# Performance work log

Measured on AMD Instinct MI355X. Metric: run time of the kernel, lower is better.

## Reference

```python
import jax, jax.numpy as jnp
import numpy as np

N, E = 50000, 800000
IN_C, HID, HEADS, NUM_CLASSES = 256, 64, 4, 10
LRELU_SLOPE = 0.2
LN_EPS = 1e-5


def setup_inputs() -> dict:
    key = jax.random.key(0)
    ks = jax.random.split(key, 12)
    HC = HEADS * HID
    glorot = lambda k, shp: jax.random.normal(k, shp, jnp.float32) * np.sqrt(2.0 / (shp[0] + shp[-1]))
    return {
        "x": jax.random.normal(ks[0], (N, IN_C), jnp.float32),
        "edge_index": jax.random.randint(ks[1], (2, E), 0, N, jnp.int64),
        "edge_weight": jax.random.uniform(ks[2], (E, 1), jnp.float32),
        "W": glorot(ks[3], (IN_C, HC)),
        "att_src": glorot(ks[4], (1, HEADS, HID)),
        "att_dst": glorot(ks[5], (1, HEADS, HID)),
        "att_edge": glorot(ks[6], (1, HEADS, HID)),
        "W_edge": glorot(ks[7], (1, HC)),
        "bias": jnp.zeros((HC,), jnp.float32),
        "ln_gamma": jnp.ones((HC,), jnp.float32),
        "ln_beta": jnp.zeros((HC,), jnp.float32),
        "fc_W": glorot(ks[8], (HC, NUM_CLASSES)),
        "fc_b": jnp.zeros((NUM_CLASSES,), jnp.float32),
    }


def reference(x, edge_index, edge_weight, W, att_src, att_dst, att_edge,
              W_edge, bias, ln_gamma, ln_beta, fc_W, fc_b):
    n = x.shape[0]
    src, dst = edge_index[0], edge_index[1]

    # GATConv: linear projection -> [N, H, C]
    xh = (x @ W).reshape(n, HEADS, HID)
    a_src = jnp.sum(xh * att_src, axis=-1)  # [N, H]
    a_dst = jnp.sum(xh * att_dst, axis=-1)  # [N, H]

    # edge feature projection (edge_dim=1) -> per-edge attention term
    eh = (edge_weight @ W_edge).reshape(-1, HEADS, HID)  # [E, H, C]
    a_edge = jnp.sum(eh * att_edge, axis=-1)             # [E, H]

    alpha = a_src[src] + a_dst[dst] + a_edge             # [E, H]
    alpha = jax.nn.leaky_relu(alpha, LRELU_SLOPE)

    # segment softmax over incoming edges of each destination node
    amax = jax.ops.segment_max(alpha, dst, num_segments=n)  # [N, H]
    amax = jnp.where(jnp.isfinite(amax), amax, 0.0)
    ex = jnp.exp(alpha - amax[dst])
    esum = jax.ops.segment_sum(ex, dst, num_segments=n)     # [N, H]
    attn = ex / (esum[dst] + 1e-16)                          # [E, H]

    # message = gathered source features weighted by attention; scatter-add
    msg = xh[src] * attn[:, :, None]                          # [E, H, C]
    out = jax.ops.segment_sum(msg, dst, num_segments=n)      # [N, H, C]
    out = out.reshape(n, HEADS * HID) + bias                  # concat heads

    # LayerNorm + ReLU (dropout is identity in eval) + Linear head
    mu = jnp.mean(out, axis=-1, keepdims=True)
    var = jnp.mean(jnp.square(out - mu), axis=-1, keepdims=True)
    out = (out - mu) * jax.lax.rsqrt(var + LN_EPS) * ln_gamma + ln_beta
    out = jax.nn.relu(out)
    return out @ fc_W + fc_b
```

## Files before the change

### kernel.cpp

```cpp
#include <hip/hip_runtime.h>
#include <hip/hip_bf16.h>

static constexpr int HEADS = 4;
static constexpr int HID   = 64;
static constexpr int HC    = 256;
static constexpr int NCLS  = 10;

typedef short    bf16x8 __attribute__((ext_vector_type(8)));
typedef _Float16 f16x8  __attribute__((ext_vector_type(8)));
typedef _Float16 f16x4  __attribute__((ext_vector_type(4)));
typedef float    f32x4  __attribute__((ext_vector_type(4)));

__device__ inline unsigned short f2bf(float f) {
    union { float f; unsigned u; } c; c.f = f;
    unsigned r = (c.u + 0x7fff + ((c.u >> 16) & 1)) >> 16;
    return (unsigned short)r;
}
__device__ inline unsigned short f2h(float f) {
    _Float16 h = (_Float16)f; unsigned short u; __builtin_memcpy(&u, &h, 2); return u;
}
__device__ inline float h2f(unsigned short u) {
    _Float16 h; __builtin_memcpy(&h, &u, 2); return (float)h;
}

__global__ void prep_kernel(const float* __restrict__ We, const float* __restrict__ attE,
                            float* __restrict__ cE, const float* __restrict__ W,
                            unsigned short* __restrict__ Wt, const float* __restrict__ fcW,
                            unsigned short* __restrict__ fcWh) {
    int b = blockIdx.x, t = threadIdx.x;
    if (b == 0) {
        float p = We[t] * attE[t];
#pragma unroll
        for (int d = 32; d; d >>= 1) p += __shfl_xor(p, d, 64);
        if ((t & 63) == 0) cE[t >> 6] = p;
    } else if (b <= 256) {
        int k = b - 1;
        Wt[t * 256 + k] = f2bf(W[k * 256 + t]);
    } else {
        int j = b - 257;
        unsigned short v = 0;
        if (j < NCLS) v = f2h(fcW[t * NCLS + j]);
        fcWh[j * 256 + t] = v;
    }
}

__global__ __launch_bounds__(256) void gemm_mfma(const float* __restrict__ X,
                                                 const unsigned short* __restrict__ Bt,
                                                 unsigned short* __restrict__ XHh, int M) {
    __shared__ alignas(16) unsigned short As[128][40];
    __shared__ alignas(16) unsigned short Bs[128][40];
    const int tid = threadIdx.x;
    const int lane = tid & 63, wid = tid >> 6;
    const int wr = wid >> 1, wc = wid & 1;
    const int bm = blockIdx.x * 128, bn = blockIdx.y * 128;
    const int fr = lane & 15, kg = lane >> 4;

    f32x4 acc[4][4] = {};

    for (int k0 = 0; k0 < 256; k0 += 32) {
        __syncthreads();
#pragma unroll
        for (int ss = 0; ss < 4; ++ss) {
            int idx = tid + (ss << 8);
            int row = idx >> 3, seg = idx & 7;
            int grow = bm + row;
            float4 av = make_float4(0.f, 0.f, 0.f, 0.f);
            if (grow < M) av = *(const float4*)&X[(size_t)grow * 256 + k0 + seg * 4];
            ushort4 ab = make_ushort4(f2bf(av.x), f2bf(av.y), f2bf(av.z), f2bf(av.w));
            *(ushort4*)&As[row][seg * 4] = ab;
        }
#pragma unroll
        for (int qq = 0; qq < 2; ++qq) {
            int q = tid + (qq << 8);
            int row = q >> 2, part = q & 3;
            const ushort4* bp = (const ushort4*)&Bt[(size_t)(bn + row) * 256 + k0 + part * 8];
            *(ushort4*)&Bs[row][part * 8]     = bp[0];
            *(ushort4*)&Bs[row][part * 8 + 4] = bp[1];
        }
        __syncthreads();

        bf16x8 af[4], bf[4];
#pragma unroll
        for (int i = 0; i < 4; ++i)
            af[i] = *(const bf16x8*)&As[wr * 64 + i * 16 + fr][kg * 8];
#pragma unroll
        for (int j = 0; j < 4; ++j)
            bf[j] = *(const bf16x8*)&Bs[wc * 64 + j * 16 + fr][kg * 8];
#pragma unroll
        for (int i = 0; i < 4; ++i)
#pragma unroll
            for (int j = 0; j < 4; ++j)
                acc[i][j] = __builtin_amdgcn_mfma_f32_16x16x32_bf16(af[i], bf[j], acc[i][j], 0, 0, 0);
    }

#pragma unroll
    for (int i = 0; i < 4; ++i) {
#pragma unroll
        for (int j = 0; j < 4; ++j) {
            int col = bn + wc * 64 + j * 16 + fr;
#pragma unroll
            for (int r = 0; r < 4; ++r) {
                int row = bm + wr * 64 + i * 16 + kg * 4 + r;
                if (row < M) XHh[(size_t)row * 256 + col] = f2h(acc[i][j][r]);
            }
        }
    }
}

__global__ __launch_bounds__(256) void attn_coef(const unsigned short* __restrict__ xhh,
                                                 const float* __restrict__ attS,
                                                 const float* __restrict__ attD,
                                                 float* __restrict__ a_src,
                                                 float* __restrict__ a_dst,
                                                 int Nn) {
    int wid = threadIdx.x >> 6, lane = threadIdx.x & 63;
    int n = blockIdx.x * 4 + wid;
    if (n >= Nn) return;
    ushort4 xv = *(const ushort4*)&xhh[(size_t)n * HC + lane * 4];
    float x0 = h2f(xv.x), x1 = h2f(xv.y), x2 = h2f(xv.z), x3 = h2f(xv.w);
    float4 sv = *(const float4*)&attS[lane * 4];
    float4 dv = *(const float4*)&attD[lane * 4];
    float ps = x0 * sv.x + x1 * sv.y + x2 * sv.z + x3 * sv.w;
    float pd = x0 * dv.x + x1 * dv.y + x2 * dv.z + x3 * dv.w;
#pragma unroll
    for (int d = 1; d < 16; d <<= 1) {
        ps += __shfl_xor(ps, d, 64);
        pd += __shfl_xor(pd, d, 64);
    }
    if ((lane & 15) == 0) {
        a_src[n * 4 + (lane >> 4)] = ps;
        a_dst[n * 4 + (lane >> 4)] = pd;
    }
}

__global__ void hist_kernel(const int* __restrict__ dst, int* __restrict__ deg,
                            int* __restrict__ rank, int E) {
    int e = blockIdx.x * 256 + threadIdx.x;
    if (e < E) rank[e] = atomicAdd(&deg[dst[e]], 1);
}

__global__ __launch_bounds__(1024) void scan1(const int* __restrict__ deg,
                                              int* __restrict__ row_start,
                                              int* __restrict__ bsum, int n) {
    __shared__ int wsum[16];
    const int tid = threadIdx.x, lane = tid & 63, wid = tid >> 6;
    int i = blockIdx.x * 1024 + tid;
    int v = (i < n) ? ((deg[i] + 3) & ~3) : 0;
    int incl = v;
#pragma unroll
    for (int d = 1; d < 64; d <<= 1) {
        int t = __shfl_up(incl, d, 64);
        if (lane >= d) incl += t;
    }
    if (lane == 63) wsum[wid] = incl;
    __syncthreads();
    if (tid < 16) {
        int w = wsum[tid];
#pragma unroll
        for (int d = 1; d < 16; d <<= 1) {
            int t = __shfl_up(w, d, 16);
            if (tid >= d) w += t;
        }
        wsum[tid] = w;
    }
    __syncthreads();
    int waveoff = wid ? wsum[wid - 1] : 0;
    if (i < n) row_start[i] = waveoff + incl - v;
    if (tid == 1023) bsum[blockIdx.x] = waveoff + incl;
}

__global__ __launch_bounds__(1024) void scan23(int* __restrict__ row_start,
                                               const int* __restrict__ bsum,
                                               const int* __restrict__ deg,
                                               int* __restrict__ srcs, int n, int nb) {
    __shared__ int pref[64];
    const int tid = threadIdx.x;
    if (tid < 64) {
        int v = (tid < nb) ? bsum[tid] : 0;
#pragma unroll
        for (int d = 1; d < 64; d <<= 1) {
            int t = __shfl_up(v, d, 64);
            if (tid >= d) v += t;
        }
        pref[tid] = v;
    }
    __syncthreads();
    int add = blockIdx.x ? pref[blockIdx.x - 1] : 0;
    int i = blockIdx.x * 1024 + tid;
    if (i < n) {
        int v = row_start[i] + add;
        row_start[i] = v;
        int dn = deg[i];
        int pd = (dn + 3) & ~3;
        for (int s = dn; s < pd; ++s) srcs[v + s] = 0;
    }
    if (i == n) row_start[n] = pref[nb - 1];
}

__global__ void scatter_sw(const int* __restrict__ src, const int* __restrict__ dst,
                           const float* __restrict__ ew,
                           const int* __restrict__ row_start, const int* __restrict__ rank,
                           int* __restrict__ srcs, float* __restrict__ ews, int E) {
    int e = blockIdx.x * 256 + threadIdx.x;
    if (e >= E) return;
    int pos = row_start[dst[e]] + rank[e];
    srcs[pos] = src[e];
    ews[pos] = ew[e];
}

__global__ __launch_bounds__(256) void p_pass(
    const int* __restrict__ row_start, const int* __restrict__ deg,
    const int* __restrict__ srcs, const float* __restrict__ ews,
    const float* __restrict__ a_src, const float* __restrict__ a_dst,
    const float* __restrict__ cE, float* __restrict__ pq, int Nn) {
    const int wid = threadIdx.x >> 6, lane = threadIdx.x & 63;
    const int n = blockIdx.x * 4 + wid;
    if (n >= Nn) return;
    const int rs = row_start[n];
    const int dn = deg[n];
    const int pd = (dn + 3) & ~3;
    const int slot0 = lane >> 2, h = lane & 3;
    const float adn = a_dst[n * 4 + h];
    const float ceh = cE[h];
    for (int s = slot0; s < pd; s += 16) {
        int pos = rs + s;
        float p = 0.f;
        if (s < dn) {
            int sv = srcs[pos];
            float w = ews[pos];
            float a = a_src[sv * 4 + h] + adn + ceh * w;
            a = fmaxf(a, 0.2f * a);
            p = __expf(a);
        }
        pq[(size_t)(pos >> 2) * 16 + h * 4 + (pos & 3)] = p;
    }
}

__global__ __launch_bounds__(256) void gat_main(
    const unsigned short* __restrict__ xhh, const int* __restrict__ row_start,
    const int* __restrict__ deg, const int* __restrict__ srcs,
    const float* __restrict__ pq, const float* __restrict__ bias,
    const float* __restrict__ gamma, const float* __restrict__ beta,
    unsigned short* __restrict__ yh, int Nn) {
    const int lane = threadIdx.x & 63, wid = threadIdx.x >> 6;
    const int n = blockIdx.x * 4 + wid;
    if (n >= Nn) return;
    const int myh = lane >> 4;
    const int rs = row_start[n];
    const int dn = deg[n];
    const int nfull = dn >> 2, rem = dn & 3;
    const unsigned short* xl = xhh + (size_t)lane * 4;

    f32x4 acc = {0.f, 0.f, 0.f, 0.f};
    float psum = 0.f;

#define LOADMETA(c, S, P)                                                     \
    S = *(const int4*)&srcs[rs + (c) * 4];                                    \
    P = *(const float4*)&pq[((size_t)((rs >> 2) + (c))) * 16 + myh * 4];
#define GATHER(S, X0, X1, X2, X3)                                             \
    X0 = *(const f16x4*)(xl + (size_t)__builtin_amdgcn_readfirstlane((S).x) * HC); \
    X1 = *(const f16x4*)(xl + (size_t)__builtin_amdgcn_readfirstlane((S).y) * HC); \
    X2 = *(const f16x4*)(xl + (size_t)__builtin_amdgcn_readfirstlane((S).z) * HC); \
    X3 = *(const f16x4*)(xl + (size_t)__builtin_amdgcn_readfirstlane((S).w) * HC);
#define COMPUTE(P, X0, X1, X2, X3)                                            \
    psum += ((P).x + (P).y) + ((P).z + (P).w);                                \
    acc[0] = fmaf((P).x, (float)(X0).x, acc[0]);                              \
    acc[1] = fmaf((P).x, (float)(X0).y, acc[1]);                              \
    acc[2] = fmaf((P).x, (float)(X0).z, acc[2]);                              \
    acc[3] = fmaf((P).x, (float)(X0).w, acc[3]);                              \
    acc[0] = fmaf((P).y, (float)(X1).x, acc[0]);                              \
    acc[1] = fmaf((P).y, (float)(X1).y, acc[1]);                              \
    acc[2] = fmaf((P).y, (float)(X1).z, acc[2]);                              \
    acc[3] = fmaf((P).y, (float)(X1).w, acc[3]);                              \
    acc[0] = fmaf((P).z, (float)(X2).x, acc[0]);                              \
    acc[1] = fmaf((P).z, (float)(X2).y, acc[1]);                              \
    acc[2] = fmaf((P).z, (float)(X2).z, acc[2]);                              \
    acc[3] = fmaf((P).z, (float)(X2).w, acc[3]);                              \
    acc[0] = fmaf((P).w, (float)(X3).x, acc[0]);                              \
    acc[1] = fmaf((P).w, (float)(X3).y, acc[1]);                              \
    acc[2] = fmaf((P).w, (float)(X3).z, acc[2]);                              \
    acc[3] = fmaf((P).w, (float)(X3).w, acc[3]);

    if (nfull > 0) {
        int4 s0, sN = {0, 0, 0, 0}, s2 = {0, 0, 0, 0};
        float4 pC, pN = {0.f, 0.f, 0.f, 0.f}, p2 = {0.f, 0.f, 0.f, 0.f};
        f16x4 g0, g1, g2, g3;
        LOADMETA(0, s0, pC);
        GATHER(s0, g0, g1, g2, g3);
        if (nfull > 1) { LOADMETA(1, sN, pN); }
        for (int c = 0; c < nfull; ++c) {
            f16x4 h0, h1, h2, h3;
            if (c + 1 < nfull) { GATHER(sN, h0, h1, h2, h3); }
            if (c + 2 < nfull) { LOADMETA(c + 2, s2, p2); }
            COMPUTE(pC, g0, g1, g2, g3);
            pC = pN; pN = p2; sN = s2;
            g0 = h0; g1 = h1; g2 = h2; g3 = h3;
        }
    }
    if (rem) {
        int4 s; float4 p;
        LOADMETA(nfull, s, p);
        p.w = 0.f;
        if (rem < 3) p.z = 0.f;
        if (rem < 2) p.y = 0.f;
        int b0 = __builtin_amdgcn_readfirstlane(s.x);
        int b1 = rem > 1 ? __builtin_amdgcn_readfirstlane(s.y) : b0;
        int b2 = rem > 2 ? __builtin_amdgcn_readfirstlane(s.z) : b0;
        f16x4 x0 = *(const f16x4*)(xl + (size_t)b0 * HC);
        f16x4 x1 = *(const f16x4*)(xl + (size_t)b1 * HC);
        f16x4 x2 = *(const f16x4*)(xl + (size_t)b2 * HC);
        COMPUTE(p, x0, x1, x2, x0);
    }
#undef LOADMETA
#undef GATHER
#undef COMPUTE

    float rin = 1.f / (psum + 1e-16f);

    float4 bv = *(const float4*)&bias[lane * 4];
    float v0 = acc[0] * rin + bv.x;
    float v1 = acc[1] * rin + bv.y;
    float v2 = acc[2] * rin + bv.z;
    float v3 = acc[3] * rin + bv.w;

    float s1 = v0 + v1 + v2 + v3;
    float s2v = v0 * v0 + v1 * v1 + v2 * v2 + v3 * v3;
#pragma unroll
    for (int d = 1; d < 64; d <<= 1) {
        s1 += __shfl_xor(s1, d, 64);
        s2v += __shfl_xor(s2v, d, 64);
    }
    float mu = s1 * (1.f / 256.f);
    float var = s2v * (1.f / 256.f) - mu * mu;
    float rstd = rsqrtf(var + 1e-5f);
    float4 gv = *(const float4*)&gamma[lane * 4];
    float4 btv = *(const float4*)&beta[lane * 4];
    float y0 = fmaxf((v0 - mu) * rstd * gv.x + btv.x, 0.f);
    float y1 = fmaxf((v1 - mu) * rstd * gv.y + btv.y, 0.f);
    float y2 = fmaxf((v2 - mu) * rstd * gv.z + btv.z, 0.f);
    float y3 = fmaxf((v3 - mu) * rstd * gv.w + btv.w, 0.f);

    f16x4 yv;
    yv.x = (_Float16)y0; yv.y = (_Float16)y1; yv.z = (_Float16)y2; yv.w = (_Float16)y3;
    *(f16x4*)&yh[(size_t)n * HC + lane * 4] = yv;
}

__global__ __launch_bounds__(256) void fc_gemm(const unsigned short* __restrict__ yh,
                                               const unsigned short* __restrict__ fcWh,
                                               const float* __restrict__ fcb,
                                               float* __restrict__ out, int M) {
    const int lane = threadIdx.x & 63, wid = threadIdx.x >> 6;
    const int rowbase = blockIdx.x * 256 + wid * 64;
    const int fr = lane & 15, kg = lane >> 4;
    f32x4 acc[4] = {};
#pragma unroll
    for (int k0 = 0; k0 < 256; k0 += 32) {
        f16x8 bfr = *(const f16x8*)&fcWh[fr * 256 + k0 + kg * 8];
#pragma unroll
        for (int i = 0; i < 4; ++i) {
            int row = rowbase + i * 16 + fr;
            f16x8 afr = {};
            if (row < M) afr = *(const f16x8*)&yh[(size_t)row * 256 + k0 + kg * 8];
            acc[i] = __builtin_amdgcn_mfma_f32_16x16x32_f16(afr, bfr, acc[i], 0, 0, 0);
        }
    }
    if (fr < NCLS) {
        float bb = fcb[fr];
#pragma unroll
        for (int i = 0; i < 4; ++i) {
#pragma unroll
            for (int r = 0; r < 4; ++r) {
                int row = rowbase + i * 16 + kg * 4 + r;
                if (row < M) out[(size_t)row * NCLS + fr] = acc[i][r] + bb;
            }
        }
    }
}

extern "C" void kernel_launch(void* const* d_in, const int* in_sizes, int n_in,
                              void* d_out, int out_size, void* d_ws, size_t ws_size,
                              hipStream_t stream) {
    const float* x    = (const float*)d_in[0];
    const int*   ei   = (const int*)d_in[1];
    const float* ew   = (const float*)d_in[2];
    const float* W    = (const float*)d_in[3];
    const float* attS = (const float*)d_in[4];
    const float* attD = (const float*)d_in[5];
    const float* attE = (const float*)d_in[6];
    const float* We   = (const float*)d_in[7];
    const float* bias = (const float*)d_in[8];
    const float* gam  = (const float*)d_in[9];
    const float* bet  = (const float*)d_in[10];
    const float* fcW  = (const float*)d_in[11];
    const float* fcb  = (const float*)d_in[12];
    float* out = (float*)d_out;

    const int Nn = in_sizes[0] / HC;
    const int E  = in_sizes[1] / 2;
    const int* src = ei;
    const int* dst = ei + E;
    const int nb = (Nn + 1023) / 1024;
    const int EpMax = E + 4 * Nn;

    char* ws = (char*)d_ws;
    size_t off = 0;
    auto alloc = [&](size_t bytes) { void* p = ws + off; off = (off + bytes + 255) & ~size_t(255); return p; };
    unsigned short* xhh  = (unsigned short*)alloc((size_t)Nn * HC * 2);
    unsigned short* yh   = (unsigned short*)alloc((size_t)Nn * HC * 2);
    unsigned short* wt   = (unsigned short*)alloc((size_t)HC * HC * 2);
    unsigned short* fcWh = (unsigned short*)alloc((size_t)16 * HC * 2);
    float* a_srcb    = (float*)alloc((size_t)Nn * 4 * 4);
    float* a_dstb    = (float*)alloc((size_t)Nn * 4 * 4);
    float* cE        = (float*)alloc(256);
    int*   row_start = (int*)  alloc((size_t)(Nn + 1) * 4);
    int*   deg       = (int*)  alloc((size_t)Nn * 4);
    int*   bsum      = (int*)  alloc((size_t)nb * 4);
    int*   rank      = (int*)  alloc((size_t)E * 4);
    int*   srcs      = (int*)  alloc((size_t)EpMax * 4 + 256);
    float* ews       = (float*)alloc((size_t)EpMax * 4 + 256);
    float* pq        = (float*)alloc((size_t)EpMax * 16 + 1024);
    (void)ws_size;

    hipMemsetAsync(deg, 0, (size_t)Nn * 4, stream);

    prep_kernel<<<273, 256, 0, stream>>>(We, attE, cE, W, wt, fcW, fcWh);

    dim3 g((Nn + 127) / 128, 2);
    gemm_mfma<<<g, 256, 0, stream>>>(x, wt, xhh, Nn);

    attn_coef<<<(Nn + 3) / 4, 256, 0, stream>>>(xhh, attS, attD, a_srcb, a_dstb, Nn);
    hist_kernel<<<(E + 255) / 256, 256, 0, stream>>>(dst, deg, rank, E);
    scan1<<<nb, 1024, 0, stream>>>(deg, row_start, bsum, Nn);
    scan23<<<nb, 1024, 0, stream>>>(row_start, bsum, deg, srcs, Nn, nb);
    scatter_sw<<<(E + 255) / 256, 256, 0, stream>>>(src, dst, ew, row_start, rank,
                                                    srcs, ews, E);
    p_pass<<<(Nn + 3) / 4, 256, 0, stream>>>(row_start, deg, srcs, ews,
                                             a_srcb, a_dstb, cE, pq, Nn);
    gat_main<<<(Nn + 3) / 4, 256, 0, stream>>>(xhh, row_start, deg, srcs, pq,
                                               bias, gam, bet, yh, Nn);
    fc_gemm<<<(Nn + 255) / 256, 256, 0, stream>>>(yh, fcWh, fcb, out, Nn);
}
```

Measured before the change: 208.0 us.

## Split GAT aggregation across two waves per node and pack edge records

```diff
diff --git a/kernel.cpp b/kernel.cpp
--- a/kernel.cpp
+++ b/kernel.cpp
@@ -26,7 +26,8 @@
 __global__ void prep_kernel(const float* __restrict__ We, const float* __restrict__ attE,
                             float* __restrict__ cE, const float* __restrict__ W,
                             unsigned short* __restrict__ Wt, const float* __restrict__ fcW,
-                            unsigned short* __restrict__ fcWh) {
+                            unsigned short* __restrict__ fcWh, int* __restrict__ deg,
+                            int Nn) {
     int b = blockIdx.x, t = threadIdx.x;
     if (b == 0) {
         float p = We[t] * attE[t];
@@ -36,11 +37,14 @@
     } else if (b <= 256) {
         int k = b - 1;
         Wt[t * 256 + k] = f2bf(W[k * 256 + t]);
-    } else {
+    } else if (b <= 272) {
         int j = b - 257;
         unsigned short v = 0;
         if (j < NCLS) v = f2h(fcW[t * NCLS + j]);
         fcWh[j * 256 + t] = v;
+    } else {
+        int i = (b - 273) * 256 + t;
+        if (i < Nn) deg[i] = 0;
     }
 }
 
@@ -172,7 +176,7 @@
 __global__ __launch_bounds__(1024) void scan23(int* __restrict__ row_start,
                                                const int* __restrict__ bsum,
                                                const int* __restrict__ deg,
-                                               int* __restrict__ srcs, int n, int nb) {
+                                               int2* __restrict__ sew, int n, int nb) {
     __shared__ int pref[64];
     const int tid = threadIdx.x;
     if (tid < 64) {
@@ -192,7 +196,7 @@
         row_start[i] = v;
         int dn = deg[i];
         int pd = (dn + 3) & ~3;
-        for (int s = dn; s < pd; ++s) srcs[v + s] = 0;
+        for (int s = dn; s < pd; ++s) sew[v + s] = make_int2(0, 0);
     }
     if (i == n) row_start[n] = pref[nb - 1];
 }
@@ -200,19 +204,18 @@
 __global__ void scatter_sw(const int* __restrict__ src, const int* __restrict__ dst,
                            const float* __restrict__ ew,
                            const int* __restrict__ row_start, const int* __restrict__ rank,
-                           int* __restrict__ srcs, float* __restrict__ ews, int E) {
+                           int2* __restrict__ sew, int E) {
     int e = blockIdx.x * 256 + threadIdx.x;
     if (e >= E) return;
     int pos = row_start[dst[e]] + rank[e];
-    srcs[pos] = src[e];
-    ews[pos] = ew[e];
+    sew[pos] = make_int2(src[e], __float_as_int(ew[e]));
 }
 
 __global__ __launch_bounds__(256) void p_pass(
     const int* __restrict__ row_start, const int* __restrict__ deg,
-    const int* __restrict__ srcs, const float* __restrict__ ews,
-    const float* __restrict__ a_src, const float* __restrict__ a_dst,
-    const float* __restrict__ cE, float* __restrict__ pq, int Nn) {
+    const int2* __restrict__ sew, const float* __restrict__ a_src,
+    const float* __restrict__ a_dst, const float* __restrict__ cE,
+    int* __restrict__ srcs, float* __restrict__ pq, int Nn) {
     const int wid = threadIdx.x >> 6, lane = threadIdx.x & 63;
     const int n = blockIdx.x * 4 + wid;
     if (n >= Nn) return;
@@ -224,39 +227,44 @@
     const float ceh = cE[h];
     for (int s = slot0; s < pd; s += 16) {
         int pos = rs + s;
+        int2 r = sew[pos];
         float p = 0.f;
         if (s < dn) {
-            int sv = srcs[pos];
-            float w = ews[pos];
-            float a = a_src[sv * 4 + h] + adn + ceh * w;
+            float a = a_src[r.x * 4 + h] + adn + ceh * __int_as_float(r.y);
             a = fmaxf(a, 0.2f * a);
             p = __expf(a);
         }
+        if (h == 0) srcs[pos] = r.x;
         pq[(size_t)(pos >> 2) * 16 + h * 4 + (pos & 3)] = p;
     }
 }
 
 __global__ __launch_bounds__(256) void gat_main(
     const unsigned short* __restrict__ xhh, const int* __restrict__ row_start,
-    const int* __restrict__ deg, const int* __restrict__ srcs,
-    const float* __restrict__ pq, const float* __restrict__ bias,
-    const float* __restrict__ gamma, const float* __restrict__ beta,
-    unsigned short* __restrict__ yh, int Nn) {
+    const int* __restrict__ srcs, const float* __restrict__ pq,
+    const float* __restrict__ bias, const float* __restrict__ gamma,
+    const float* __restrict__ beta, unsigned short* __restrict__ yh, int Nn) {
+    __shared__ alignas(16) f32x4 s_acc[2][64];
+    __shared__ float s_ps[2][64];
+
     const int lane = threadIdx.x & 63, wid = threadIdx.x >> 6;
-    const int n = blockIdx.x * 4 + wid;
-    if (n >= Nn) return;
+    const int nslot = wid >> 1, sub = wid & 1;
+    const int n = blockIdx.x * 2 + nslot;
     const int myh = lane >> 4;
-    const int rs = row_start[n];
-    const int dn = deg[n];
-    const int nfull = dn >> 2, rem = dn & 3;
     const unsigned short* xl = xhh + (size_t)lane * 4;
 
     f32x4 acc = {0.f, 0.f, 0.f, 0.f};
     float psum = 0.f;
 
+    if (n < Nn) {
+        const int rs = row_start[n], re = row_start[n + 1];
+        const int rs4 = rs >> 2;
+        const int G = (re - rs) >> 2;
+        const int myG = (G - sub + 1) >> 1;
+
 #define LOADMETA(c, S, P)                                                     \
-    S = *(const int4*)&srcs[rs + (c) * 4];                                    \
-    P = *(const float4*)&pq[((size_t)((rs >> 2) + (c))) * 16 + myh * 4];
+    S = *(const int4*)&srcs[(rs4 + (c)) * 4];                                 \
+    P = *(const float4*)&pq[((size_t)(rs4 + (c))) * 16 + myh * 4];
 #define GATHER(S, X0, X1, X2, X3)                                             \
     X0 = *(const f16x4*)(xl + (size_t)__builtin_amdgcn_readfirstlane((S).x) * HC); \
     X1 = *(const f16x4*)(xl + (size_t)__builtin_amdgcn_readfirstlane((S).y) * HC); \
@@ -281,39 +289,33 @@
     acc[2] = fmaf((P).w, (float)(X3).z, acc[2]);                              \
     acc[3] = fmaf((P).w, (float)(X3).w, acc[3]);
 
-    if (nfull > 0) {
-        int4 s0, sN = {0, 0, 0, 0}, s2 = {0, 0, 0, 0};
-        float4 pC, pN = {0.f, 0.f, 0.f, 0.f}, p2 = {0.f, 0.f, 0.f, 0.f};
-        f16x4 g0, g1, g2, g3;
-        LOADMETA(0, s0, pC);
-        GATHER(s0, g0, g1, g2, g3);
-        if (nfull > 1) { LOADMETA(1, sN, pN); }
-        for (int c = 0; c < nfull; ++c) {
-            f16x4 h0, h1, h2, h3;
-            if (c + 1 < nfull) { GATHER(sN, h0, h1, h2, h3); }
-            if (c + 2 < nfull) { LOADMETA(c + 2, s2, p2); }
-            COMPUTE(pC, g0, g1, g2, g3);
-            pC = pN; pN = p2; sN = s2;
-            g0 = h0; g1 = h1; g2 = h2; g3 = h3;
-        }
-    }
-    if (rem) {
-        int4 s; float4 p;
-        LOADMETA(nfull, s, p);
-        p.w = 0.f;
-        if (rem < 3) p.z = 0.f;
-        if (rem < 2) p.y = 0.f;
-        int b0 = __builtin_amdgcn_readfirstlane(s.x);
-        int b1 = rem > 1 ? __builtin_amdgcn_readfirstlane(s.y) : b0;
-        int b2 = rem > 2 ? __builtin_amdgcn_readfirstlane(s.z) : b0;
-        f16x4 x0 = *(const f16x4*)(xl + (size_t)b0 * HC);
-        f16x4 x1 = *(const f16x4*)(xl + (size_t)b1 * HC);
-        f16x4 x2 = *(const f16x4*)(xl + (size_t)b2 * HC);
-        COMPUTE(p, x0, x1, x2, x0);
-    }
+        if (myG > 0) {
+            int4 s0, sN = {0, 0, 0, 0}, s2 = {0, 0, 0, 0};
+            float4 pC, pN = {0.f, 0.f, 0.f, 0.f}, p2 = {0.f, 0.f, 0.f, 0.f};
+            f16x4 g0, g1, g2, g3;
+            LOADMETA(sub, s0, pC);
+            GATHER(s0, g0, g1, g2, g3);
+            if (myG > 1) { LOADMETA(sub + 2, sN, pN); }
+            for (int k = 0; k < myG; ++k) {
+                f16x4 h0, h1, h2, h3;
+                if (k + 1 < myG) { GATHER(sN, h0, h1, h2, h3); }
+                if (k + 2 < myG) { LOADMETA(sub + 2 * (k + 2), s2, p2); }
+                COMPUTE(pC, g0, g1, g2, g3);
+                pC = pN; pN = p2; sN = s2;
+                g0 = h0; g1 = h1; g2 = h2; g3 = h3;
+            }
+        }
 #undef LOADMETA
 #undef GATHER
 #undef COMPUTE
+    }
+
+    if (sub == 1) { s_acc[nslot][lane] = acc; s_ps[nslot][lane] = psum; }
+    __syncthreads();
+    if (sub == 1 || n >= Nn) return;
+    f32x4 oacc = s_acc[nslot][lane];
+    acc[0] += oacc[0]; acc[1] += oacc[1]; acc[2] += oacc[2]; acc[3] += oacc[3];
+    psum += s_ps[nslot][lane];
 
     float rin = 1.f / (psum + 1e-16f);
 
@@ -416,14 +418,13 @@
     int*   deg       = (int*)  alloc((size_t)Nn * 4);
     int*   bsum      = (int*)  alloc((size_t)nb * 4);
     int*   rank      = (int*)  alloc((size_t)E * 4);
+    int2*  sew       = (int2*) alloc((size_t)EpMax * 8 + 256);
     int*   srcs      = (int*)  alloc((size_t)EpMax * 4 + 256);
-    float* ews       = (float*)alloc((size_t)EpMax * 4 + 256);
     float* pq        = (float*)alloc((size_t)EpMax * 16 + 1024);
     (void)ws_size;
 
-    hipMemsetAsync(deg, 0, (size_t)Nn * 4, stream);
-
-    prep_kernel<<<273, 256, 0, stream>>>(We, attE, cE, W, wt, fcW, fcWh);
+    prep_kernel<<<273 + (Nn + 255) / 256, 256, 0, stream>>>(We, attE, cE, W, wt,
+                                                            fcW, fcWh, deg, Nn);
 
     dim3 g((Nn + 127) / 128, 2);
     gemm_mfma<<<g, 256, 0, stream>>>(x, wt, xhh, Nn);
@@ -431,12 +432,12 @@
     attn_coef<<<(Nn + 3) / 4, 256, 0, stream>>>(xhh, attS, attD, a_srcb, a_dstb, Nn);
     hist_kernel<<<(E + 255) / 256, 256, 0, stream>>>(dst, deg, rank, E);
     scan1<<<nb, 1024, 0, stream>>>(deg, row_start, bsum, Nn);
-    scan23<<<nb, 1024, 0, stream>>>(row_start, bsum, deg, srcs, Nn, nb);
+    scan23<<<nb, 1024, 0, stream>>>(row_start, bsum, deg, sew, Nn, nb);
     scatter_sw<<<(E + 255) / 256, 256, 0, stream>>>(src, dst, ew, row_start, rank,
-                                                    srcs, ews, E);
-    p_pass<<<(Nn + 3) / 4, 256, 0, stream>>>(row_start, deg, srcs, ews,
-                                             a_srcb, a_dstb, cE, pq, Nn);
-    gat_main<<<(Nn + 3) / 4, 256, 0, stream>>>(xhh, row_start, deg, srcs, pq,
+                                                    sew, E);
+    p_pass<<<(Nn + 3) / 4, 256, 0, stream>>>(row_start, deg, sew,
+                                             a_srcb, a_dstb, cE, srcs, pq, Nn);
+    gat_main<<<(Nn + 1) / 2, 256, 0, stream>>>(xhh, row_start, srcs, pq,
                                                bias, gam, bet, yh, Nn);
     fc_gemm<<<(Nn + 255) / 256, 256, 0, stream>>>(yh, fcWh, fcb, out, Nn);
 }
```

Result: faster. 198.8 us (-4.4%).
